# Kernel tuning notes

Measured on AMD Instinct MI355X. Metric: run time of the kernel, lower is better.

Reference implementation:

```python
import jax, jax.numpy as jnp
import numpy as np

EMBED = 1024
HEADS = 16
HEAD_DIM = EMBED // HEADS


def setup_inputs() -> dict:
    key = jax.random.key(0)
    ks = jax.random.split(key, 10)
    B, S = 2, 2048
    x = jax.random.normal(ks[0], (B, S, EMBED), dtype=jnp.float32)
    s = 1.0 / np.sqrt(EMBED)
    Wq = jax.random.normal(ks[1], (EMBED, EMBED), dtype=jnp.float32) * s
    Wk = jax.random.normal(ks[2], (EMBED, EMBED), dtype=jnp.float32) * s
    Wv = jax.random.normal(ks[3], (EMBED, EMBED), dtype=jnp.float32) * s
    Wo = jax.random.normal(ks[4], (EMBED, EMBED), dtype=jnp.float32) * s
    bq = jnp.zeros((EMBED,), jnp.float32)
    bk = jnp.zeros((EMBED,), jnp.float32)
    bv = jnp.zeros((EMBED,), jnp.float32)
    bo = jnp.zeros((EMBED,), jnp.float32)
    J = jax.random.normal(ks[5], (HEADS, HEAD_DIM, HEAD_DIM), dtype=jnp.float32) * 0.02
    lam = jnp.asarray(0.5, jnp.float32)
    return {"x": x, "Wq": Wq, "bq": bq, "Wk": Wk, "bk": bk,
            "Wv": Wv, "bv": bv, "Wo": Wo, "bo": bo, "J": J, "lam": lam}


def reference(x, Wq, bq, Wk, bk, Wv, bv, Wo, bo, J, lam):
    B, S, E = x.shape
    H, hd = HEADS, HEAD_DIM
    scale = np.sqrt(hd).astype(np.float32)

    def split_heads(t):  # (B,S,E) -> (B,H,S,hd)
        return t.reshape(B, S, H, hd).transpose(0, 2, 1, 3)

    Q = split_heads(x @ Wq + bq)
    K = split_heads(x @ Wk + bk)
    V = split_heads(x @ Wv + bv)

    scores = jnp.einsum('bhid,bhjd->bhij', Q, K) / scale
    Qn = jnp.tanh(Q)
    Kn = jnp.tanh(K)
    # bilinear correction: tanh(Q) J tanh(K)^T per head
    delta = jnp.einsum('bhid,hde,bhje->bhij', Qn, J, Kn)
    scores = scores + lam * delta

    causal = jnp.triu(jnp.ones((S, S), dtype=bool), k=1)  # True above diagonal
    scores = jnp.where(causal[None, None], -jnp.inf, scores)

    probs = jax.nn.softmax(scores, axis=-1)
    out = jnp.einsum('bhij,bhjd->bhid', probs, V)
    out = out.transpose(0, 2, 1, 3).reshape(B, S, E)
    return out @ Wo + bo
```

## Files before the change

kernel.cpp:

```cpp
#include <hip/hip_runtime.h>
#include <cstdint>
#include <cstddef>

typedef __bf16 bf16x8 __attribute__((ext_vector_type(8)));
typedef short  s16x8  __attribute__((ext_vector_type(8)));
typedef float  f32x4  __attribute__((ext_vector_type(4)));
typedef unsigned int u32x4 __attribute__((ext_vector_type(4)));

#define MFMA16(a, b, c) __builtin_amdgcn_mfma_f32_16x16x32_bf16((a), (b), (c), 0, 0, 0)

typedef __attribute__((address_space(3))) unsigned int       lds_uint;
typedef const __attribute__((address_space(1))) unsigned int glb_uint;

static __device__ __forceinline__ void gload_lds16(const void* g, void* l) {
  __builtin_amdgcn_global_load_lds((glb_uint*)g, (lds_uint*)l, 16, 0, 0);
}

static __device__ __forceinline__ unsigned short f2bf(float f) {
  unsigned u = __builtin_bit_cast(unsigned, f);
  unsigned r = u + 0x7FFFu + ((u >> 16) & 1u);
  return (unsigned short)(r >> 16);
}
static __device__ __forceinline__ float bf2f(unsigned short u) {
  unsigned x = ((unsigned)u) << 16;
  return __builtin_bit_cast(float, x);
}
static __device__ __forceinline__ float fast_tanh(float x) {
  float e = __expf(2.f * x);
  return 1.f - 2.f / (e + 1.f);
}
static __device__ __forceinline__ unsigned cvt_pk_bf16(float lo, float hi) {
  unsigned r;
  asm("v_cvt_pk_bf16_f32 %0, %1, %2" : "=v"(r) : "v"(lo), "v"(hi));
  return r;
}

__global__ void k_f32_to_bf16(const float* __restrict__ src,
                              unsigned short* __restrict__ dst, int n4) {
  int i = blockIdx.x * blockDim.x + threadIdx.x;
  if (i >= n4) return;
  float4 v = reinterpret_cast<const float4*>(src)[i];
  ushort4 o;
  o.x = f2bf(v.x); o.y = f2bf(v.y); o.z = f2bf(v.z); o.w = f2bf(v.w);
  reinterpret_cast<ushort4*>(dst)[i] = o;
}

__global__ void k_transpose_to_bf16(const float* __restrict__ src,
                                    unsigned short* __restrict__ dst,
                                    int Rr, int Cc) {
  __shared__ float t[32][33];
  int c0 = blockIdx.x * 32, r0 = blockIdx.y * 32;
  int tx = threadIdx.x, ty = threadIdx.y;
#pragma unroll
  for (int i = 0; i < 4; ++i)
    t[ty + i * 8][tx] = src[(size_t)(r0 + ty + i * 8) * Cc + c0 + tx];
  __syncthreads();
#pragma unroll
  for (int i = 0; i < 4; ++i)
    dst[(size_t)(c0 + ty + i * 8) * Rr + r0 + tx] = f2bf(t[tx][ty + i * 8]);
}

template <int MODE>
__global__ __launch_bounds__(256) void k_gemm(
    const unsigned short* __restrict__ A, const unsigned short* __restrict__ Bt,
    int M, int N, int K,
    float* __restrict__ Cout, const float* __restrict__ bias,
    const float* __restrict__ bq, const float* __restrict__ bk,
    const float* __restrict__ bv,
    unsigned short* __restrict__ Qa, unsigned short* __restrict__ Ka,
    unsigned short* __restrict__ Vt, unsigned short* __restrict__ Qn) {
  __shared__ __align__(16) unsigned short Al[128 * 64];
  __shared__ __align__(16) unsigned short Bl[128 * 64];
  const int tid = threadIdx.x;
  const int lane = tid & 63, w = tid >> 6;
  const int wm = w >> 1, wn = w & 1;
  const int l15 = lane & 15, l4 = lane >> 4;
  const int m0 = blockIdx.y * 128, n0 = blockIdx.x * 128;

  const int srow = lane >> 3;
  const int schunk = (lane & 7) ^ srow;
  const unsigned short* Ag = A + (size_t)(m0 + (w << 5) + srow) * K + (schunk << 3);
  const unsigned short* Bg = Bt + (size_t)(n0 + (w << 5) + srow) * K + (schunk << 3);
  unsigned short* Alw = Al + (w << 5) * 64;
  unsigned short* Blw = Bl + (w << 5) * 64;

  const f32x4 zero4 = {0.f, 0.f, 0.f, 0.f};
  f32x4 acc[4][4];
#pragma unroll
  for (int i = 0; i < 4; ++i)
#pragma unroll
    for (int j = 0; j < 4; ++j) acc[i][j] = zero4;

  for (int k0 = 0; k0 < K; k0 += 64) {
#pragma unroll
    for (int p = 0; p < 4; ++p) {
      gload_lds16(Ag + (size_t)(p * 8) * K + k0, Alw + p * 8 * 64);
      gload_lds16(Bg + (size_t)(p * 8) * K + k0, Blw + p * 8 * 64);
    }
    __syncthreads();
#pragma unroll
    for (int c = 0; c < 2; ++c) {
      bf16x8 af[4], bfr[4];
#pragma unroll
      for (int i = 0; i < 4; ++i) {
        int ra = wm * 64 + i * 16 + l15;
        af[i] = *reinterpret_cast<const bf16x8*>(
            reinterpret_cast<const char*>(Al) + ra * 128 +
            ((c * 64 + l4 * 16) ^ ((ra & 7) << 4)));
        int rb = wn * 64 + i * 16 + l15;
        bfr[i] = *reinterpret_cast<const bf16x8*>(
            reinterpret_cast<const char*>(Bl) + rb * 128 +
            ((c * 64 + l4 * 16) ^ ((rb & 7) << 4)));
      }
#pragma unroll
      for (int i = 0; i < 4; ++i)
#pragma unroll
        for (int j = 0; j < 4; ++j) acc[i][j] = MFMA16(af[i], bfr[j], acc[i][j]);
    }
    __syncthreads();
  }

#pragma unroll
  for (int i = 0; i < 4; ++i) {
#pragma unroll
    for (int j = 0; j < 4; ++j) {
#pragma unroll
      for (int r = 0; r < 4; ++r) {
        int mrow = m0 + wm * 64 + i * 16 + l4 * 4 + r;
        int ncol = n0 + wn * 64 + j * 16 + l15;
        float v = acc[i][j][r];
        if (MODE == 0) {
          Cout[(size_t)mrow * N + ncol] = v + bias[ncol];
        } else {
          int proj = ncol >> 10, nn = ncol & 1023;
          int h = nn >> 6, d = nn & 63;
          int b = mrow >> 11, s = mrow & 2047;
          size_t t64 = (size_t)(b * 16 + h) * 2048 + s;
          if (proj == 0) {
            float q = v + bq[nn];
            Qa[t64 * 128 + d] = f2bf(q * 0.125f);
            Qn[t64 * 64 + d] = f2bf(fast_tanh(q));
          } else if (proj == 1) {
            float kk = v + bk[nn];
            Ka[t64 * 128 + d] = f2bf(kk);
            Ka[t64 * 128 + 64 + d] = f2bf(fast_tanh(kk));
          } else {
            Vt[((size_t)(b * 16 + h) * 64 + d) * 2048 + s] = f2bf(v + bv[nn]);
          }
        }
      }
    }
  }
}

__global__ __launch_bounds__(256) void k_qnj(const unsigned short* __restrict__ Qn,
                                             const float* __restrict__ J,
                                             const float* __restrict__ lamPtr,
                                             unsigned short* __restrict__ Qa) {
  __shared__ float Jl[64 * 64];
  __shared__ float Ql[64 * 64];
  int bid = blockIdx.x;
  int bh = bid >> 5, sblk = bid & 31;
  int h = bh & 15;
  int tid = threadIdx.x;
  float lam = lamPtr[0];
  const float4* Jh = reinterpret_cast<const float4*>(J + (size_t)h * 4096);
#pragma unroll
  for (int p = 0; p < 4; ++p)
    reinterpret_cast<float4*>(Jl)[p * 256 + tid] = Jh[p * 256 + tid];
  size_t tok0 = (size_t)bh * 2048 + sblk * 64;
#pragma unroll
  for (int p = 0; p < 2; ++p) {
    int idx = p * 256 + tid;
    s16x8 v = *reinterpret_cast<const s16x8*>(Qn + tok0 * 64 + idx * 8);
#pragma unroll
    for (int j = 0; j < 8; ++j) Ql[idx * 8 + j] = bf2f((unsigned short)v[j]);
  }
  __syncthreads();
  int e = tid & 63, wq = tid >> 6;
#pragma unroll 1
  for (int pass = 0; pass < 16; ++pass) {
    int tok = pass * 4 + wq;
    float a0 = 0.f, a1 = 0.f;
#pragma unroll
    for (int d = 0; d < 64; d += 2) {
      a0 += Ql[tok * 64 + d] * Jl[d * 64 + e];
      a1 += Ql[tok * 64 + d + 1] * Jl[(d + 1) * 64 + e];
    }
    Qa[(tok0 + tok) * 128 + 64 + e] = f2bf(lam * (a0 + a1));
  }
}

__global__ __launch_bounds__(256) void k_attn(const unsigned short* __restrict__ Qa,
                                              const unsigned short* __restrict__ Ka,
                                              const unsigned short* __restrict__ Vt,
                                              unsigned short* __restrict__ Ob) {
  constexpr int S = 2048;
  __shared__ __align__(16) unsigned short Klds[2][64 * 128];
  __shared__ __align__(16) unsigned short Vtl[2][64 * 64];

  const int blk = (int)blockIdx.x;
  const int xg = blk & 7, idx = blk >> 3;
  const int bh = xg * 4 + (idx & 3);
  const int qt = 31 - (idx >> 2);
  const int b = bh >> 4, h = bh & 15;
  const int tid = threadIdx.x;
  const int lane = tid & 63, w = tid >> 6;
  const int l15 = lane & 15, l4 = lane >> 4;
  const int q0 = qt * 64;
  const size_t bhS = (size_t)bh * S;
  const unsigned short* Kbase = Ka + bhS * 128;
  const unsigned short* Vbase = Vt + (size_t)bh * 64 * 2048;
  const f32x4 zero4 = {0.f, 0.f, 0.f, 0.f};

  const int rowbase = w * 16 + (lane >> 4);
  const int rb7 = rowbase & 7;
  const int cK0 = (lane & 15) ^ rb7;
  const int cK1 = cK0 ^ 4;
  const int vdvrow = w * 16 + (lane >> 3);
  const int cV = (lane & 7) ^ ((lane >> 3) & 7);

  bf16x8 qf[4];
  {
    int qrow = q0 + w * 16 + l15;
#pragma unroll
    for (int c = 0; c < 4; ++c)
      qf[c] = *reinterpret_cast<const bf16x8*>(Qa + (bhS + qrow) * 128 + c * 32 + l4 * 8);
  }

  f32x4 oacc[4];
  float m_ = -__builtin_inff(), lsum = 0.f;
#pragma unroll
  for (int v = 0; v < 4; ++v) oacc[v] = zero4;

  const int I0 = (l15 + 32 * (l4 & 1)) * 4;
  const int I1 = I0 + 64;
  const bool hi4 = (lane & 32) != 0;

#pragma unroll
  for (int p = 0; p < 4; ++p)
    gload_lds16(Kbase + (size_t)(rowbase + 4 * p) * 128 + ((p & 1) ? cK1 : cK0) * 8,
                &Klds[0][(w * 16 + p * 4) * 128]);
#pragma unroll
  for (int p = 0; p < 2; ++p)
    gload_lds16(Vbase + (size_t)(vdvrow + 8 * p) * 2048 + cV * 8,
                &Vtl[0][(w * 16 + p * 8) * 64]);
  __syncthreads();

  for (int kt = 0; kt <= qt; ++kt) {
    const int cur = kt & 1;
    const bool lastStep = (kt == qt);

    if (!lastStep) {
      const int base = (kt + 1) * 64;
      const int nxt = cur ^ 1;
#pragma unroll
      for (int p = 0; p < 4; ++p)
        gload_lds16(Kbase + (size_t)(base + rowbase + 4 * p) * 128 + ((p & 1) ? cK1 : cK0) * 8,
                    &Klds[nxt][(w * 16 + p * 4) * 128]);
#pragma unroll
      for (int p = 0; p < 2; ++p)
        gload_lds16(Vbase + (size_t)(vdvrow + 8 * p) * 2048 + base + cV * 8,
                    &Vtl[nxt][(w * 16 + p * 8) * 64]);
    }

    const char* Kl = reinterpret_cast<const char*>(Klds[cur]);
    f32x4 sc[4];
    __builtin_amdgcn_s_setprio(1);
#pragma unroll
    for (int fn = 0; fn < 4; ++fn) {
      sc[fn] = zero4;
      const int krow = fn * 16 + l15;
#pragma unroll
      for (int c = 0; c < 4; ++c) {
        bf16x8 kf = *reinterpret_cast<const bf16x8*>(
            Kl + krow * 256 + (((c * 4 + l4) ^ (krow & 7)) << 4));
        sc[fn] = MFMA16(kf, qf[c], sc[fn]);
      }
    }
    __builtin_amdgcn_s_setprio(0);

    if (lastStep) {
      const int qloc = w * 16 + l15;
#pragma unroll
      for (int fn = 0; fn < 4; ++fn)
#pragma unroll
        for (int r = 0; r < 4; ++r)
          if (fn * 16 + l4 * 4 + r > qloc) sc[fn][r] = -__builtin_inff();
    }

    float mx = sc[0][0];
#pragma unroll
    for (int fn = 0; fn < 4; ++fn)
#pragma unroll
      for (int r = 0; r < 4; ++r) mx = fmaxf(mx, sc[fn][r]);
    mx = fmaxf(mx, __shfl_xor(mx, 16));
    mx = fmaxf(mx, __shfl_xor(mx, 32));
    const float mn = fmaxf(m_, mx);
    const float al = __expf(m_ - mn);
    float p_[4][4];
    float rs = 0.f;
#pragma unroll
    for (int fn = 0; fn < 4; ++fn)
#pragma unroll
      for (int r = 0; r < 4; ++r) {
        float e = __expf(sc[fn][r] - mn);
        p_[fn][r] = e;
        rs += e;
      }
    rs += __shfl_xor(rs, 16);
    rs += __shfl_xor(rs, 32);
    lsum = lsum * al + rs;
    m_ = mn;

#pragma unroll
    for (int r = 0; r < 4; ++r) {
      float albc = __shfl(al, l4 * 4 + r);
#pragma unroll
      for (int v = 0; v < 4; ++v) oacc[v][r] *= albc;
    }

    unsigned cp[4][2];
#pragma unroll
    for (int fn = 0; fn < 4; ++fn) {
      cp[fn][0] = cvt_pk_bf16(p_[fn][0], p_[fn][1]);
      cp[fn][1] = cvt_pk_bf16(p_[fn][2], p_[fn][3]);
    }

    const char* Vl = reinterpret_cast<const char*>(Vtl[cur]);
#pragma unroll
    for (int c2 = 0; c2 < 2; ++c2) {
      unsigned a0 = __builtin_amdgcn_ds_bpermute(I0, (int)cp[c2 * 2][0]);
      unsigned b0 = __builtin_amdgcn_ds_bpermute(I0, (int)cp[c2 * 2 + 1][0]);
      unsigned a1 = __builtin_amdgcn_ds_bpermute(I0, (int)cp[c2 * 2][1]);
      unsigned b1 = __builtin_amdgcn_ds_bpermute(I0, (int)cp[c2 * 2 + 1][1]);
      unsigned a2 = __builtin_amdgcn_ds_bpermute(I1, (int)cp[c2 * 2][0]);
      unsigned b2 = __builtin_amdgcn_ds_bpermute(I1, (int)cp[c2 * 2 + 1][0]);
      unsigned a3 = __builtin_amdgcn_ds_bpermute(I1, (int)cp[c2 * 2][1]);
      unsigned b3 = __builtin_amdgcn_ds_bpermute(I1, (int)cp[c2 * 2 + 1][1]);
      u32x4 pw = {hi4 ? b0 : a0, hi4 ? b1 : a1, hi4 ? b2 : a2, hi4 ? b3 : a3};
      bf16x8 pa = __builtin_bit_cast(bf16x8, pw);
      __builtin_amdgcn_s_setprio(1);
#pragma unroll
      for (int v = 0; v < 4; ++v) {
        const int dvrow = v * 16 + l15;
        bf16x8 vf = *reinterpret_cast<const bf16x8*>(
            Vl + dvrow * 128 + (((c2 * 4 + l4) ^ (dvrow & 7)) << 4));
        oacc[v] = MFMA16(pa, vf, oacc[v]);
      }
      __builtin_amdgcn_s_setprio(0);
    }

    __syncthreads();
  }

  float lbc[4];
#pragma unroll
  for (int r = 0; r < 4; ++r) lbc[r] = __shfl(lsum, l4 * 4 + r);
#pragma unroll
  for (int v = 0; v < 4; ++v) {
#pragma unroll
    for (int r = 0; r < 4; ++r) {
      int row = q0 + w * 16 + l4 * 4 + r;
      float o = oacc[v][r] / lbc[r];
      Ob[((size_t)b * S + row) * 1024 + h * 64 + v * 16 + l15] = f2bf(o);
    }
  }
}

extern "C" void kernel_launch(void* const* d_in, const int* in_sizes, int n_in,
                              void* d_out, int out_size, void* d_ws, size_t ws_size,
                              hipStream_t stream) {
  const float* x   = (const float*)d_in[0];
  const float* Wq  = (const float*)d_in[1];
  const float* bq  = (const float*)d_in[2];
  const float* Wk  = (const float*)d_in[3];
  const float* bk  = (const float*)d_in[4];
  const float* Wv  = (const float*)d_in[5];
  const float* bv  = (const float*)d_in[6];
  const float* Wo  = (const float*)d_in[7];
  const float* bo  = (const float*)d_in[8];
  const float* J   = (const float*)d_in[9];
  const float* lam = (const float*)d_in[10];
  float* out = (float*)d_out;

  char* ws = (char*)d_ws;
  unsigned short* xb     = (unsigned short*)(ws);
  unsigned short* Wt_qkv = (unsigned short*)(ws + 8388608);
  unsigned short* Wt_o   = (unsigned short*)(ws + 14680064);
  unsigned short* Qa     = (unsigned short*)(ws + 16777216);
  unsigned short* Ka     = (unsigned short*)(ws + 33554432);
  unsigned short* Vt     = (unsigned short*)(ws + 50331648);
  unsigned short* Qn     = (unsigned short*)(ws + 58720256);
  unsigned short* Ob     = (unsigned short*)(ws + 67108864);

  k_f32_to_bf16<<<4096, 256, 0, stream>>>(x, xb, 1048576);

  dim3 tb(32, 8), tg(32, 32);
  k_transpose_to_bf16<<<tg, tb, 0, stream>>>(Wq, Wt_qkv + 0,       1024, 1024);
  k_transpose_to_bf16<<<tg, tb, 0, stream>>>(Wk, Wt_qkv + 1048576, 1024, 1024);
  k_transpose_to_bf16<<<tg, tb, 0, stream>>>(Wv, Wt_qkv + 2097152, 1024, 1024);
  k_transpose_to_bf16<<<tg, tb, 0, stream>>>(Wo, Wt_o,             1024, 1024);

  k_gemm<1><<<dim3(24, 32), 256, 0, stream>>>(xb, Wt_qkv, 4096, 3072, 1024,
      nullptr, nullptr, bq, bk, bv, Qa, Ka, Vt, Qn);

  k_qnj<<<1024, 256, 0, stream>>>(Qn, J, lam, Qa);

  k_attn<<<1024, 256, 0, stream>>>(Qa, Ka, Vt, Ob);

  k_gemm<0><<<dim3(8, 32), 256, 0, stream>>>(Ob, Wt_o, 4096, 1024, 1024,
      out, bo, nullptr, nullptr, nullptr, nullptr, nullptr, nullptr, nullptr);
}
```

Baseline: 197.7 us.

## Replace QKV projection GEMM with 256x256-tile double-buffered pipelined kernel

Adds a dedicated QKV projection kernel with 256x256 output tiles, 8 waves per block, and double-buffered LDS. Global-to-LDS loads for the next K tile are interleaved with four MFMA quadrants, using explicit barriers, waitcnts and setprio. A block-index swizzle groups blocks for better L2 reuse. The larger tile cuts global traffic per FLOP, but only 192 blocks are launched (under one wave on 256 CUs), and the hand-tuned synchronization adds complexity.

New measurement: 196.6 us, median of 2. No clear change (-0.6%).

```diff
diff --git a/kernel.cpp b/kernel.cpp
--- a/kernel.cpp
+++ b/kernel.cpp
@@ -64,11 +64,7 @@
 __global__ __launch_bounds__(256) void k_gemm(
     const unsigned short* __restrict__ A, const unsigned short* __restrict__ Bt,
     int M, int N, int K,
-    float* __restrict__ Cout, const float* __restrict__ bias,
-    const float* __restrict__ bq, const float* __restrict__ bk,
-    const float* __restrict__ bv,
-    unsigned short* __restrict__ Qa, unsigned short* __restrict__ Ka,
-    unsigned short* __restrict__ Vt, unsigned short* __restrict__ Qn) {
+    float* __restrict__ Cout, const float* __restrict__ bias) {
   __shared__ __align__(16) unsigned short Al[128 * 64];
   __shared__ __align__(16) unsigned short Bl[128 * 64];
   const int tid = threadIdx.x;
@@ -121,32 +117,185 @@
   }
 
 #pragma unroll
-  for (int i = 0; i < 4; ++i) {
-#pragma unroll
-    for (int j = 0; j < 4; ++j) {
+  for (int i = 0; i < 4; ++i)
+#pragma unroll
+    for (int j = 0; j < 4; ++j)
 #pragma unroll
       for (int r = 0; r < 4; ++r) {
         int mrow = m0 + wm * 64 + i * 16 + l4 * 4 + r;
         int ncol = n0 + wn * 64 + j * 16 + l15;
-        float v = acc[i][j][r];
-        if (MODE == 0) {
-          Cout[(size_t)mrow * N + ncol] = v + bias[ncol];
+        Cout[(size_t)mrow * N + ncol] = acc[i][j][r] + bias[ncol];
+      }
+}
+
+__global__ __launch_bounds__(512, 2) void k_gemm256_qkv(
+    const unsigned short* __restrict__ A, const unsigned short* __restrict__ Bt,
+    int M, int N, int K,
+    const float* __restrict__ bq, const float* __restrict__ bk,
+    const float* __restrict__ bv,
+    unsigned short* __restrict__ Qa, unsigned short* __restrict__ Ka,
+    unsigned short* __restrict__ Vt, unsigned short* __restrict__ Qn) {
+  __shared__ __align__(16) unsigned short Al[2][256 * 64];
+  __shared__ __align__(16) unsigned short Bl[2][256 * 64];
+  const int tid = threadIdx.x;
+  const int lane = tid & 63;
+  const int w = tid >> 6, wm = w >> 2, wn = w & 3;
+  const int l15 = lane & 15, l4 = lane >> 4;
+  const int nbx = N >> 8;
+  const int bid = (int)blockIdx.x;
+  const int lin = (bid & 7) * ((int)gridDim.x >> 3) + (bid >> 3);
+  const int m0 = (lin / nbx) << 8, n0 = (lin % nbx) << 8;
+  const int NT = K >> 6;
+
+  const int strow = tid >> 3, stchunk = tid & 7;
+  const int schunk = stchunk ^ (strow & 7);
+
+  auto stage = [&](int slot, int kt, int hh) {
+    const unsigned short* src = (hh < 2) ? A : Bt;
+    const int base0 = (hh < 2) ? m0 : n0;
+    unsigned short* dst = (hh < 2) ? &Al[slot][0] : &Bl[slot][0];
+    const int hrow = (hh & 1) * 128;
+#pragma unroll
+    for (int i = 0; i < 2; ++i) {
+      int row = hrow + i * 64 + strow;
+      gload_lds16(src + (size_t)(base0 + row) * K + kt * 64 + schunk * 8,
+                  dst + row * 64 + stchunk * 8);
+    }
+  };
+
+  const f32x4 zero4 = {0.f, 0.f, 0.f, 0.f};
+  f32x4 acc[8][4];
+#pragma unroll
+  for (int i = 0; i < 8; ++i)
+#pragma unroll
+    for (int j = 0; j < 4; ++j) acc[i][j] = zero4;
+
+  stage(0, 0, 0); stage(0, 0, 1); stage(0, 0, 2); stage(0, 0, 3);
+  stage(1, 1, 0);
+  asm volatile("s_waitcnt vmcnt(2)" ::: "memory");
+  __builtin_amdgcn_s_barrier();
+
+  bf16x8 af[4][2], bf0[2][2], bf1[2][2];
+
+  for (int kt = 0; kt < NT; ++kt) {
+    const int s = kt & 1;
+    const char* As = (const char*)&Al[s][0];
+    const char* Bs = (const char*)&Bl[s][0];
+    const int kp1 = (kt + 1 < NT) ? kt + 1 : NT - 1;
+    const int kp2 = (kt + 2 < NT) ? kt + 2 : NT - 1;
+
+#pragma unroll
+    for (int i = 0; i < 4; ++i) {
+      const int ra = wm * 128 + i * 16 + l15;
+#pragma unroll
+      for (int kk = 0; kk < 2; ++kk)
+        af[i][kk] = *(const bf16x8*)(As + ra * 128 + (((kk * 4 + l4) ^ (ra & 7)) << 4));
+    }
+#pragma unroll
+    for (int j = 0; j < 2; ++j) {
+      const int rb = wn * 64 + j * 16 + l15;
+#pragma unroll
+      for (int kk = 0; kk < 2; ++kk)
+        bf0[j][kk] = *(const bf16x8*)(Bs + rb * 128 + (((kk * 4 + l4) ^ (rb & 7)) << 4));
+    }
+    stage(s ^ 1, kp1, 1);
+    __builtin_amdgcn_s_barrier();
+    asm volatile("s_waitcnt lgkmcnt(0)" ::: "memory");
+    __builtin_amdgcn_sched_barrier(0);
+    __builtin_amdgcn_s_setprio(1);
+#pragma unroll
+    for (int i = 0; i < 4; ++i)
+#pragma unroll
+      for (int j = 0; j < 2; ++j)
+#pragma unroll
+        for (int kk = 0; kk < 2; ++kk)
+          acc[i][j] = MFMA16(af[i][kk], bf0[j][kk], acc[i][j]);
+    __builtin_amdgcn_s_setprio(0);
+    __builtin_amdgcn_s_barrier();
+
+#pragma unroll
+    for (int j = 0; j < 2; ++j) {
+      const int rb = wn * 64 + (2 + j) * 16 + l15;
+#pragma unroll
+      for (int kk = 0; kk < 2; ++kk)
+        bf1[j][kk] = *(const bf16x8*)(Bs + rb * 128 + (((kk * 4 + l4) ^ (rb & 7)) << 4));
+    }
+    stage(s ^ 1, kp1, 2);
+    __builtin_amdgcn_s_barrier();
+    asm volatile("s_waitcnt lgkmcnt(0)" ::: "memory");
+    __builtin_amdgcn_sched_barrier(0);
+    __builtin_amdgcn_s_setprio(1);
+#pragma unroll
+    for (int i = 0; i < 4; ++i)
+#pragma unroll
+      for (int j = 0; j < 2; ++j)
+#pragma unroll
+        for (int kk = 0; kk < 2; ++kk)
+          acc[i][2 + j] = MFMA16(af[i][kk], bf1[j][kk], acc[i][2 + j]);
+    __builtin_amdgcn_s_setprio(0);
+    __builtin_amdgcn_s_barrier();
+
+#pragma unroll
+    for (int i = 0; i < 4; ++i) {
+      const int ra = wm * 128 + (4 + i) * 16 + l15;
+#pragma unroll
+      for (int kk = 0; kk < 2; ++kk)
+        af[i][kk] = *(const bf16x8*)(As + ra * 128 + (((kk * 4 + l4) ^ (ra & 7)) << 4));
+    }
+    stage(s ^ 1, kp1, 3);
+    __builtin_amdgcn_s_barrier();
+    asm volatile("s_waitcnt lgkmcnt(0)" ::: "memory");
+    __builtin_amdgcn_sched_barrier(0);
+    __builtin_amdgcn_s_setprio(1);
+#pragma unroll
+    for (int i = 0; i < 4; ++i)
+#pragma unroll
+      for (int j = 0; j < 2; ++j)
+#pragma unroll
+        for (int kk = 0; kk < 2; ++kk)
+          acc[4 + i][2 + j] = MFMA16(af[i][kk], bf1[j][kk], acc[4 + i][2 + j]);
+    __builtin_amdgcn_s_setprio(0);
+    __builtin_amdgcn_s_barrier();
+
+    stage(s, kp2, 0);
+    asm volatile("s_waitcnt vmcnt(2)" ::: "memory");
+    __builtin_amdgcn_s_barrier();
+    __builtin_amdgcn_s_setprio(1);
+#pragma unroll
+    for (int i = 0; i < 4; ++i)
+#pragma unroll
+      for (int j = 0; j < 2; ++j)
+#pragma unroll
+        for (int kk = 0; kk < 2; ++kk)
+          acc[4 + i][j] = MFMA16(af[i][kk], bf0[j][kk], acc[4 + i][j]);
+    __builtin_amdgcn_s_setprio(0);
+    __builtin_amdgcn_s_barrier();
+  }
+  asm volatile("s_waitcnt vmcnt(0)" ::: "memory");
+
+#pragma unroll
+  for (int mf = 0; mf < 8; ++mf) {
+#pragma unroll
+    for (int nf = 0; nf < 4; ++nf) {
+#pragma unroll
+      for (int r = 0; r < 4; ++r) {
+        const int mrow = m0 + wm * 128 + mf * 16 + l4 * 4 + r;
+        const int ncol = n0 + wn * 64 + nf * 16 + l15;
+        const float v = acc[mf][nf][r];
+        const int proj = ncol >> 10, nn = ncol & 1023;
+        const int h = nn >> 6, d = nn & 63;
+        const int b = mrow >> 11, sq = mrow & 2047;
+        const size_t t64 = (size_t)(b * 16 + h) * 2048 + sq;
+        if (proj == 0) {
+          float q = v + bq[nn];
+          Qa[t64 * 128 + d] = f2bf(q * 0.125f);
+          Qn[t64 * 64 + d] = f2bf(fast_tanh(q));
+        } else if (proj == 1) {
+          float kk = v + bk[nn];
+          Ka[t64 * 128 + d] = f2bf(kk);
+          Ka[t64 * 128 + 64 + d] = f2bf(fast_tanh(kk));
         } else {
-          int proj = ncol >> 10, nn = ncol & 1023;
-          int h = nn >> 6, d = nn & 63;
-          int b = mrow >> 11, s = mrow & 2047;
-          size_t t64 = (size_t)(b * 16 + h) * 2048 + s;
-          if (proj == 0) {
-            float q = v + bq[nn];
-            Qa[t64 * 128 + d] = f2bf(q * 0.125f);
-            Qn[t64 * 64 + d] = f2bf(fast_tanh(q));
-          } else if (proj == 1) {
-            float kk = v + bk[nn];
-            Ka[t64 * 128 + d] = f2bf(kk);
-            Ka[t64 * 128 + 64 + d] = f2bf(fast_tanh(kk));
-          } else {
-            Vt[((size_t)(b * 16 + h) * 64 + d) * 2048 + s] = f2bf(v + bv[nn]);
-          }
+          Vt[((size_t)(b * 16 + h) * 64 + d) * 2048 + sq] = f2bf(v + bv[nn]);
         }
       }
     }
@@ -402,13 +551,13 @@
   k_transpose_to_bf16<<<tg, tb, 0, stream>>>(Wv, Wt_qkv + 2097152, 1024, 1024);
   k_transpose_to_bf16<<<tg, tb, 0, stream>>>(Wo, Wt_o,             1024, 1024);
 
-  k_gemm<1><<<dim3(24, 32), 256, 0, stream>>>(xb, Wt_qkv, 4096, 3072, 1024,
-      nullptr, nullptr, bq, bk, bv, Qa, Ka, Vt, Qn);
+  k_gemm256_qkv<<<192, 512, 0, stream>>>(xb, Wt_qkv, 4096, 3072, 1024,
+      bq, bk, bv, Qa, Ka, Vt, Qn);
 
   k_qnj<<<1024, 256, 0, stream>>>(Qn, J, lam, Qa);
 
   k_attn<<<1024, 256, 0, stream>>>(Qa, Ka, Vt, Ob);
 
   k_gemm<0><<<dim3(8, 32), 256, 0, stream>>>(Ob, Wt_o, 4096, 1024, 1024,
-      out, bo, nullptr, nullptr, nullptr, nullptr, nullptr, nullptr, nullptr);
-}
+      out, bo);
+}
```
